# Kernel tuning notes

Measured on AMD Instinct MI355X. Metric: run time of the kernel, lower is better.

Reference implementation:

```python
import jax, jax.numpy as jnp
import numpy as np

BATCH = 256
MAX_STEP = 200
NUM_Q = 1000


def setup_inputs() -> dict:
    key = jax.random.key(0)
    k1, k2 = jax.random.split(key)
    # predictions strictly inside (0, 1) for BCE
    pred = jax.random.uniform(k1, (BATCH, MAX_STEP - 1, NUM_Q), dtype=jnp.float32) * 0.98 + 0.01
    # sparse binary error-ID labels; some rows all-zero -> masked out (ragged structure)
    batch = (jax.random.uniform(k2, (BATCH, MAX_STEP, NUM_Q)) < 0.002).astype(jnp.float32)
    # guarantee every student has at least one attempted row (torch BCE on empty -> NaN)
    batch = batch.at[:, 1, 0].set(1.0)
    return {"pred": pred, "batch": batch}


def reference(pred, batch):
    # ErrorIDs path: gt = batch[student][1:], keep rows containing any 1.
    gt = batch[:, 1:, :]                              # [B, T-1, Q]
    row_mask = jnp.any(gt == 1.0, axis=-1)            # [B, T-1] ragged mask
    m = row_mask[:, :, None].astype(pred.dtype)       # [B, T-1, 1]

    # nn.BCELoss: -(y*log(p) + (1-y)*log(1-p)), logs clamped at -100, mean reduction
    log_p = jnp.maximum(jnp.log(pred), -100.0)
    log_1mp = jnp.maximum(jnp.log1p(-pred), -100.0)
    bce = -(gt * log_p + (1.0 - gt) * log_1mp)        # [B, T-1, Q]

    n_elem = row_mask.sum(axis=1).astype(pred.dtype) * gt.shape[-1]  # selected elements per student
    per_student = (bce * m).sum(axis=(1, 2)) / n_elem               # mean BCE per student
    loss = per_student.sum()                                        # summed over students

    # Original returns ragged concatenations of selected rows; we return the
    # equivalent masked full tensors plus the row mask (same information, jit-friendly).
    return (loss, pred * m, gt * m, row_mask)
```

## Files before the change

kernel.cpp:

```cpp
#include <hip/hip_runtime.h>

#define BATCHN 256
#define TSTEPS 199
#define NQ     1000
#define NROWS  (BATCHN * TSTEPS)

__global__ void zero_ws_kernel(float* __restrict__ ws) {
    int i = threadIdx.x;
    if (i < 2 * BATCHN) ws[i] = 0.0f;
}

__global__ __launch_bounds__(256) void main_kernel(
    const float* __restrict__ pred,
    const float* __restrict__ batch,
    float* __restrict__ out,
    float* __restrict__ ws)
{
    const int r = blockIdx.x;
    const int b = r / TSTEPS;
    const int t = r - b * TSTEPS;
    const int i = threadIdx.x;

    const float4* p4 = (const float4*)(pred + (size_t)r * NQ);
    const float4* g4 = (const float4*)(batch + ((size_t)b * 200 + t + 1) * NQ);

    float4 p = make_float4(0.f, 0.f, 0.f, 0.f);
    float4 g = make_float4(0.f, 0.f, 0.f, 0.f);
    if (i < 250) { p = p4[i]; g = g4[i]; }

    float s = 0.0f;
    int any = 0;
    if (i < 250) {
        float pe[4] = {p.x, p.y, p.z, p.w};
        float ge[4] = {g.x, g.y, g.z, g.w};
        #pragma unroll
        for (int k = 0; k < 4; ++k) {
            any |= (ge[k] == 1.0f);
            float lp = fmaxf(__logf(pe[k]),        -100.0f);
            float l1 = fmaxf(__logf(1.0f - pe[k]), -100.0f);
            s -= l1 + ge[k] * (lp - l1);
        }
    }

    #pragma unroll
    for (int off = 32; off > 0; off >>= 1) {
        s   += __shfl_down(s, off);
        any |= __shfl_down(any, off);
    }

    __shared__ float ssum[4];
    __shared__ int   sany[4];
    const int lane = i & 63, wid = i >> 6;
    if (lane == 0) { ssum[wid] = s; sany[wid] = any; }
    __syncthreads();

    __shared__ float bsum;
    __shared__ int   bany;
    if (i == 0) {
        bsum = ssum[0] + ssum[1] + ssum[2] + ssum[3];
        bany = sany[0] | sany[1] | sany[2] | sany[3];
    }
    __syncthreads();

    const float m = bany ? 1.0f : 0.0f;

    float* out_pred = out + 1;
    float* out_gt   = out + 1 + (size_t)NROWS * NQ;
    float* out_mask = out + 1 + 2 * (size_t)NROWS * NQ;

    if (i < 250) {
        size_t o = (size_t)r * NQ + 4 * (size_t)i;
        out_pred[o + 0] = p.x * m;
        out_pred[o + 1] = p.y * m;
        out_pred[o + 2] = p.z * m;
        out_pred[o + 3] = p.w * m;
        out_gt[o + 0] = g.x * m;
        out_gt[o + 1] = g.y * m;
        out_gt[o + 2] = g.z * m;
        out_gt[o + 3] = g.w * m;
    }
    if (i == 0) {
        out_mask[r] = m;
        if (bany) {
            atomicAdd(&ws[b], bsum);
            atomicAdd(&ws[BATCHN + b], 1.0f);
        }
    }
}

__global__ __launch_bounds__(256) void final_kernel(
    float* __restrict__ out, const float* __restrict__ ws)
{
    const int b = threadIdx.x;
    float per = ws[b] / (ws[BATCHN + b] * (float)NQ);

    #pragma unroll
    for (int off = 32; off > 0; off >>= 1) per += __shfl_down(per, off);

    __shared__ float ssum[4];
    const int lane = b & 63, wid = b >> 6;
    if (lane == 0) ssum[wid] = per;
    __syncthreads();
    if (b == 0) out[0] = ssum[0] + ssum[1] + ssum[2] + ssum[3];
}

extern "C" void kernel_launch(void* const* d_in, const int* in_sizes, int n_in,
                              void* d_out, int out_size, void* d_ws, size_t ws_size,
                              hipStream_t stream) {
    const float* pred  = (const float*)d_in[0];
    const float* batch = (const float*)d_in[1];
    float* out = (float*)d_out;
    float* ws  = (float*)d_ws;

    zero_ws_kernel<<<1, 512, 0, stream>>>(ws);
    main_kernel<<<NROWS, 256, 0, stream>>>(pred, batch, out, ws);
    final_kernel<<<1, 256, 0, stream>>>(out, ws);
}
```

Before: 698.6 us.

## Assign one row per wavefront with ballot mask and nontemporal loads/stores

Each 64-lane wavefront now processes a whole row, with four float4 loads per lane instead of one per thread, and each block covers four rows. The block-wide shared-memory reductions and both __syncthreads are replaced by a wave ballot for the row mask and a shuffle reduction for the sum. Loads and stores use nontemporal builtins to avoid cache pollution in this streaming kernel. Outputs are still written as scalar nontemporal stores, which may not merge into wide stores, and the grid shrinks fourfold.

```diff
diff --git a/kernel.cpp b/kernel.cpp
--- a/kernel.cpp
+++ b/kernel.cpp
@@ -4,6 +4,9 @@
 #define TSTEPS 199
 #define NQ     1000
 #define NROWS  (BATCHN * TSTEPS)
+#define ROW4   250
+
+typedef float v4f __attribute__((ext_vector_type(4)));
 
 __global__ void zero_ws_kernel(float* __restrict__ ws) {
     int i = threadIdx.x;
@@ -16,73 +19,70 @@
     float* __restrict__ out,
     float* __restrict__ ws)
 {
-    const int r = blockIdx.x;
+    const int lane = threadIdx.x & 63;
+    const int wib  = threadIdx.x >> 6;
+    const int r = blockIdx.x * 4 + wib;
     const int b = r / TSTEPS;
     const int t = r - b * TSTEPS;
-    const int i = threadIdx.x;
 
-    const float4* p4 = (const float4*)(pred + (size_t)r * NQ);
-    const float4* g4 = (const float4*)(batch + ((size_t)b * 200 + t + 1) * NQ);
+    const v4f* p4 = (const v4f*)(pred + (size_t)r * NQ);
+    const v4f* g4 = (const v4f*)(batch + ((size_t)b * 200 + t + 1) * NQ);
 
-    float4 p = make_float4(0.f, 0.f, 0.f, 0.f);
-    float4 g = make_float4(0.f, 0.f, 0.f, 0.f);
-    if (i < 250) { p = p4[i]; g = g4[i]; }
+    v4f p[4], g[4];
+    #pragma unroll
+    for (int k = 0; k < 4; ++k) {
+        const int idx = lane + 64 * k;
+        if (k < 3 || idx < ROW4) {
+            p[k] = __builtin_nontemporal_load(&p4[idx]);
+            g[k] = __builtin_nontemporal_load(&g4[idx]);
+        } else {
+            p[k] = (v4f)(0.0f);
+            g[k] = (v4f)(0.0f);
+        }
+    }
 
     float s = 0.0f;
     int any = 0;
-    if (i < 250) {
-        float pe[4] = {p.x, p.y, p.z, p.w};
-        float ge[4] = {g.x, g.y, g.z, g.w};
+    #pragma unroll
+    for (int k = 0; k < 4; ++k) {
         #pragma unroll
-        for (int k = 0; k < 4; ++k) {
-            any |= (ge[k] == 1.0f);
-            float lp = fmaxf(__logf(pe[k]),        -100.0f);
-            float l1 = fmaxf(__logf(1.0f - pe[k]), -100.0f);
-            s -= l1 + ge[k] * (lp - l1);
+        for (int j = 0; j < 4; ++j) {
+            const float pe = p[k][j];
+            const float ge = g[k][j];
+            any |= (ge == 1.0f);
+            float lp = fmaxf(__logf(pe),        -100.0f);
+            float l1 = fmaxf(__logf(1.0f - pe), -100.0f);
+            s -= l1 + ge * (lp - l1);
         }
     }
 
+    const unsigned long long bal = __ballot(any != 0);
+    const float m = bal ? 1.0f : 0.0f;
+
     #pragma unroll
-    for (int off = 32; off > 0; off >>= 1) {
-        s   += __shfl_down(s, off);
-        any |= __shfl_down(any, off);
-    }
-
-    __shared__ float ssum[4];
-    __shared__ int   sany[4];
-    const int lane = i & 63, wid = i >> 6;
-    if (lane == 0) { ssum[wid] = s; sany[wid] = any; }
-    __syncthreads();
-
-    __shared__ float bsum;
-    __shared__ int   bany;
-    if (i == 0) {
-        bsum = ssum[0] + ssum[1] + ssum[2] + ssum[3];
-        bany = sany[0] | sany[1] | sany[2] | sany[3];
-    }
-    __syncthreads();
-
-    const float m = bany ? 1.0f : 0.0f;
+    for (int off = 32; off > 0; off >>= 1) s += __shfl_down(s, off);
 
     float* out_pred = out + 1;
     float* out_gt   = out + 1 + (size_t)NROWS * NQ;
     float* out_mask = out + 1 + 2 * (size_t)NROWS * NQ;
 
-    if (i < 250) {
-        size_t o = (size_t)r * NQ + 4 * (size_t)i;
-        out_pred[o + 0] = p.x * m;
-        out_pred[o + 1] = p.y * m;
-        out_pred[o + 2] = p.z * m;
-        out_pred[o + 3] = p.w * m;
-        out_gt[o + 0] = g.x * m;
-        out_gt[o + 1] = g.y * m;
-        out_gt[o + 2] = g.z * m;
-        out_gt[o + 3] = g.w * m;
+    #pragma unroll
+    for (int k = 0; k < 4; ++k) {
+        const int idx = lane + 64 * k;
+        if (k < 3 || idx < ROW4) {
+            const size_t o = (size_t)r * NQ + 4 * (size_t)idx;
+            #pragma unroll
+            for (int j = 0; j < 4; ++j) {
+                __builtin_nontemporal_store(p[k][j] * m, &out_pred[o + j]);
+                __builtin_nontemporal_store(g[k][j] * m, &out_gt[o + j]);
+            }
+        }
     }
-    if (i == 0) {
-        out_mask[r] = m;
-        if (bany) {
-            atomicAdd(&ws[b], bsum);
+
+    if (lane == 0) {
+        __builtin_nontemporal_store(m, &out_mask[r]);
+        if (bal) {
+            atomicAdd(&ws[b], s);
             atomicAdd(&ws[BATCHN + b], 1.0f);
         }
     }
@@ -113,6 +113,6 @@
     float* ws  = (float*)d_ws;
 
     zero_ws_kernel<<<1, 512, 0, stream>>>(ws);
-    main_kernel<<<NROWS, 256, 0, stream>>>(pred, batch, out, ws);
+    main_kernel<<<NROWS / 4, 256, 0, stream>>>(pred, batch, out, ws);
     final_kernel<<<1, 256, 0, stream>>>(out, ws);
 }
```

Measured after the change: 702.9 us. Within noise of the previous version (+0.6%).
